# Optimization experiments

Hardware: AMD Instinct MI355X
Metric: run time of the kernel (lower is better)

Reference implementation:

```python
import jax, jax.numpy as jnp
import numpy as np
from jax import lax
from jax.scipy.special import ndtri
from jax.scipy.stats import norm

# Hyperparameters from __init__ defaults (num_inputs=8)
MU_A = 0.99          # sigmoid(logit_mu_a)
SIGMA_A = 0.1
A_MAX = 1.0          # truncation upper bound (module-level constant in repo)
SIGMASQ0 = 1.0       # initial-state variance (module-level constant in repo)
SIGMA_MU_X = 1.0
MU_W = 0.0
SIGMA_W = 1.0

S, T, D = 512, 8192, 8


def setup_inputs() -> dict:
    key = jax.random.key(0)
    ks = jax.random.split(key, 8)
    return dict(
        inputs=jax.random.normal(ks[0], (S, T, D), jnp.float32),
        eps_w=jax.random.normal(ks[1], (S, D), jnp.float32),
        u_a=jax.random.uniform(ks[2], (S,), jnp.float32, 1e-4, 1.0 - 1e-4),
        sigmasq=jax.random.uniform(ks[3], (S,), jnp.float32, 0.01, 0.3),
        eps_mu=jax.random.normal(ks[4], (S,), jnp.float32),
        eps_x0=jax.random.normal(ks[5], (S,), jnp.float32),
        eps_x=jax.random.normal(ks[6], (S, T), jnp.float32),
        u_bern=jax.random.uniform(ks[7], (S, T), jnp.float32),
    )


def reference(inputs, eps_w, u_a, sigmasq, eps_mu, eps_x0, eps_x, u_bern):
    # Per-subject parameter draws (reparameterized)
    w = MU_W + SIGMA_W * eps_w                              # [S, D]  Normal(mu_w, sigma_w)
    # TruncatedNormal(MU_A, SIGMA_A, 0, A_MAX) via inverse CDF
    alpha = (0.0 - MU_A) / SIGMA_A
    beta = (A_MAX - MU_A) / SIGMA_A
    Fa, Fb = norm.cdf(alpha), norm.cdf(beta)
    a = MU_A + SIGMA_A * ndtri(Fa + u_a * (Fb - Fa))        # [S]
    mu_x = SIGMA_MU_X * eps_mu                              # [S]  Normal(0, sigma_mu_x)
    b = mu_x * (1.0 - a)                                    # [S]
    x0 = mu_x + jnp.sqrt(SIGMASQ0) * eps_x0                 # [S]
    sd = jnp.sqrt(sigmasq)                                  # [S]

    # AR(1) latent scan over trials, vectorized over subjects.
    # Matches original: outputs collect x_t BEFORE the update, i.e. x_0..x_{T-1}.
    def step(x, eps_t):
        x_next = a * x + b + sd * eps_t
        return x_next, x

    _, xs = lax.scan(step, x0, eps_x.T)                     # xs: [T, S]
    x = xs.T                                                # [S, T]

    logits = x + jnp.einsum('std,sd->st', inputs, w)        # [S, T]
    y = (u_bern < jax.nn.sigmoid(logits)).astype(jnp.int32) # Bernoulli(logits) sample
    return x, y
```

## Files before the change

### kernel.cpp

```cpp
#include <hip/hip_runtime.h>
#include <cmath>

#define S_SUB 512
#define T_TR  8192
#define D_IN  8
#define NSEG  4
#define SEGT  (T_TR/NSEG)
#define BLK   256
#define CH    (SEGT/BLK)
#define NW    (BLK/64)

typedef float f4 __attribute__((ext_vector_type(4)));

__device__ __forceinline__ void param_chain(double Fa, double dF,
    float ua, float sq, float emu, float ex0,
    double& a, double& b, double& sd, double& x0)
{
    const double RS2 = 0.7071067811865476;
    const double S2  = 1.4142135623730951;
    const double ISQ = 0.3989422804014327;
    double p = fma((double)ua, dF, Fa);
    double z = -S2 * erfcinv(2.0 * p);
    #pragma unroll
    for (int it = 0; it < 2; ++it) {
        double F   = 0.5 * erfc(-z * RS2);
        double pdf = exp(-0.5 * z * z) * ISQ;
        z -= (F - p) / pdf;
    }
    a  = 0.99 + 0.1 * z;
    double mu = (double)emu;
    b  = mu * (1.0 - a);
    x0 = mu + (double)ex0;
    sd = sqrt((double)sq);
}

__global__ __launch_bounds__(BLK) void compose_kernel(
    const float* __restrict__ eps_x,
    const float* __restrict__ u_a,
    const float* __restrict__ sigmasq,
    const float* __restrict__ eps_mu,
    const float* __restrict__ eps_x0,
    double Fa, double dF,
    double2* __restrict__ comp,
    double* __restrict__ params)
{
    const int bid = blockIdx.x;
    const int s   = bid >> 2;
    const int seg = bid & 3;
    if (seg == NSEG - 1) return;
    const int tid  = threadIdx.x;
    const int lane = tid & 63;
    const int wid  = tid >> 6;

    __shared__ double  pl[3];
    __shared__ double2 wtot[NW];

    const size_t base = (size_t)s * T_TR + (size_t)seg * SEGT + (size_t)tid * CH;

    const f4* e4 = (const f4*)(eps_x + base);
    f4 v0 = e4[0];
    f4 v1 = e4[1];

    if (tid < 64) {
        double a, b, sd, x0;
        param_chain(Fa, dF, u_a[s], sigmasq[s], eps_mu[s], eps_x0[s], a, b, sd, x0);
        if (tid == 0) {
            pl[0] = a; pl[1] = b; pl[2] = sd;
            if (seg == 0) {
                params[4*s+0] = a;  params[4*s+1] = b;
                params[4*s+2] = sd; params[4*s+3] = x0;
            }
        }
    }
    __syncthreads();
    const double a = pl[0], b = pl[1], sd = pl[2];

    float ev[CH];
    ev[0]=v0.x; ev[1]=v0.y; ev[2]=v0.z; ev[3]=v0.w;
    ev[4]=v1.x; ev[5]=v1.y; ev[6]=v1.z; ev[7]=v1.w;

    double A = 1.0, Bv = 0.0;
    #pragma unroll
    for (int j = 0; j < CH; ++j) {
        double c = fma(sd, (double)ev[j], b);
        Bv = fma(a, Bv, c);
        A *= a;
    }

    #pragma unroll
    for (int off = 1; off < 64; off <<= 1) {
        double pA = __shfl_down(A, off);
        double pB = __shfl_down(Bv, off);
        Bv = fma(pA, Bv, pB);
        A  = pA * A;
    }
    if (lane == 0) wtot[wid] = make_double2(A, Bv);
    __syncthreads();
    if (tid == 0) {
        double CA = wtot[0].x, CB = wtot[0].y;
        #pragma unroll
        for (int w = 1; w < NW; ++w) {
            CB = fma(wtot[w].x, CB, wtot[w].y);
            CA = wtot[w].x * CA;
        }
        comp[seg * S_SUB + s] = make_double2(CA, CB);
    }
}

__global__ __launch_bounds__(BLK, 8) void fused_kernel(
    const float* __restrict__ inputs,
    const float* __restrict__ eps_w,
    const float* __restrict__ eps_x,
    const float* __restrict__ u_bern,
    const double* __restrict__ params,
    const double2* __restrict__ comp,
    float* __restrict__ out_x,
    float* __restrict__ out_y)
{
    const int bid  = blockIdx.x;
    const int s    = bid >> 2;
    const int seg  = bid & 3;
    const int tid  = threadIdx.x;
    const int lane = tid & 63;
    const int wid  = tid >> 6;

    __shared__ double2 wtot[NW];
    __shared__ double  xs[BLK * (CH + 1)];

    const size_t segbase = (size_t)s * T_TR + (size_t)seg * SEGT;
    const size_t base    = segbase + (size_t)tid * CH;

    const f4* e4 = (const f4*)(eps_x + base);
    f4 ev0 = e4[0];
    f4 ev1 = e4[1];

    const double a  = params[4*s+0];
    const double b  = params[4*s+1];
    const double sd = params[4*s+2];
    double xseed    = params[4*s+3];
    for (int i = 0; i < seg; ++i) {
        double2 c = comp[i * S_SUB + s];
        xseed = fma(c.x, xseed, c.y);
    }

    const float* wp = eps_w + s * D_IN;
    const double w0 = (double)wp[0], w1 = (double)wp[1];
    const double w2 = (double)wp[2], w3 = (double)wp[3];
    const double w4 = (double)wp[4], w5 = (double)wp[5];
    const double w6 = (double)wp[6], w7 = (double)wp[7];

    float ev[CH];
    ev[0]=ev0.x; ev[1]=ev0.y; ev[2]=ev0.z; ev[3]=ev0.w;
    ev[4]=ev1.x; ev[5]=ev1.y; ev[6]=ev1.z; ev[7]=ev1.w;

    double A = 1.0, Bv = 0.0;
    #pragma unroll
    for (int j = 0; j < CH; ++j) {
        double c = fma(sd, (double)ev[j], b);
        Bv = fma(a, Bv, c);
        A *= a;
    }

    #pragma unroll
    for (int off = 1; off < 64; off <<= 1) {
        double pA = __shfl_up(A, off);
        double pB = __shfl_up(Bv, off);
        if (lane >= off) {
            Bv = fma(A, pB, Bv);
            A  = A * pA;
        }
    }
    if (lane == 63) wtot[wid] = make_double2(A, Bv);
    __syncthreads();

    double PA = 1.0, PB = 0.0;
    for (int w = 0; w < wid; ++w) {
        double2 t = wtot[w];
        PB = fma(t.x, PB, t.y);
        PA = t.x * PA;
    }
    double eA = __shfl_up(A, 1);
    double eB = __shfl_up(Bv, 1);
    if (lane == 0) { eA = 1.0; eB = 0.0; }
    double EB = fma(eA, PB, eB);
    double EA = eA * PA;
    double x  = fma(EA, xseed, EB);

    #pragma unroll
    for (int j = 0; j < CH; ++j) {
        xs[tid * (CH + 1) + j] = x;
        double c = fma(sd, (double)ev[j], b);
        x = fma(a, x, c);
    }
    __syncthreads();

    float uv[CH];
    #pragma unroll
    for (int j = 0; j < CH; ++j)
        uv[j] = u_bern[segbase + j * BLK + tid];

    const f4* in4 = (const f4*)(inputs + segbase * D_IN);
    #pragma unroll
    for (int j = 0; j < CH; ++j) {
        const int t = j * BLK + tid;
        f4 i0 = in4[2*t];
        f4 i1 = in4[2*t + 1];
        double xv = xs[(t >> 3) * (CH + 1) + (t & 7)];
        double dot = fma((double)i0.x, w0,
                     fma((double)i0.y, w1,
                     fma((double)i0.z, w2,
                     fma((double)i0.w, w3,
                     fma((double)i1.x, w4,
                     fma((double)i1.y, w5,
                     fma((double)i1.z, w6, (double)i1.w * w7)))))));
        double L = xv + dot;
        double E = exp(-L);
        out_y[segbase + t] = ((double)uv[j] * (1.0 + E) < 1.0) ? 1.0f : 0.0f;
        out_x[segbase + t] = (float)xv;
    }
}

extern "C" void kernel_launch(void* const* d_in, const int* in_sizes, int n_in,
                              void* d_out, int out_size, void* d_ws, size_t ws_size,
                              hipStream_t stream) {
    const float* inputs  = (const float*)d_in[0];
    const float* eps_w   = (const float*)d_in[1];
    const float* u_a     = (const float*)d_in[2];
    const float* sigmasq = (const float*)d_in[3];
    const float* eps_mu  = (const float*)d_in[4];
    const float* eps_x0  = (const float*)d_in[5];
    const float* eps_x   = (const float*)d_in[6];
    const float* u_bern  = (const float*)d_in[7];

    float* out = (float*)d_out;

    double*  params = (double*)d_ws;
    double2* comp   = (double2*)((char*)d_ws + 16*1024);

    const double RS2 = 0.7071067811865476;
    const double Fa  = 0.5 * erfc(9.9 * RS2);
    const double Fb  = 0.5 * erfc(-0.1 * RS2);
    const double dF  = Fb - Fa;

    compose_kernel<<<S_SUB*NSEG, BLK, 0, stream>>>(eps_x, u_a, sigmasq, eps_mu,
                                                   eps_x0, Fa, dF, comp, params);
    fused_kernel<<<S_SUB*NSEG, BLK, 0, stream>>>(inputs, eps_w, eps_x, u_bern,
                                                 params, comp,
                                                 out, out + (size_t)S_SUB * T_TR);
}
```

Before: 41.12 us.

## Fold segment-carry composition into main kernel, move param setup to tiny kernel

Replaces the compose kernel, which launched 2048 blocks to reduce earlier segments, with a small setup kernel that only computes per-subject AR parameters. The main kernel now recomputes the composed affine transform of all preceding segments itself, by reading their eps_x slices and doing a block reduction. This removes a large kernel launch and the comp workspace round-trip. In exchange, later segments redo up to three segments' worth of reads and reductions, plus extra block barriers, so work is uneven across blocks.

```diff
diff --git a/kernel.cpp b/kernel.cpp
--- a/kernel.cpp
+++ b/kernel.cpp
@@ -12,14 +12,18 @@
 
 typedef float f4 __attribute__((ext_vector_type(4)));
 
-__device__ __forceinline__ void param_chain(double Fa, double dF,
-    float ua, float sq, float emu, float ex0,
-    double& a, double& b, double& sd, double& x0)
-{
+__global__ void setup_kernel(const float* __restrict__ u_a,
+                             const float* __restrict__ sigmasq,
+                             const float* __restrict__ eps_mu,
+                             const float* __restrict__ eps_x0,
+                             double Fa, double dF,
+                             double* __restrict__ params) {
+    int s = blockIdx.x * blockDim.x + threadIdx.x;
+    if (s >= S_SUB) return;
     const double RS2 = 0.7071067811865476;
     const double S2  = 1.4142135623730951;
     const double ISQ = 0.3989422804014327;
-    double p = fma((double)ua, dF, Fa);
+    double p = fma((double)u_a[s], dF, Fa);
     double z = -S2 * erfcinv(2.0 * p);
     #pragma unroll
     for (int it = 0; it < 2; ++it) {
@@ -27,93 +31,23 @@
         double pdf = exp(-0.5 * z * z) * ISQ;
         z -= (F - p) / pdf;
     }
-    a  = 0.99 + 0.1 * z;
-    double mu = (double)emu;
-    b  = mu * (1.0 - a);
-    x0 = mu + (double)ex0;
-    sd = sqrt((double)sq);
+    double a  = 0.99 + 0.1 * z;
+    double mu = (double)eps_mu[s];
+    double b  = mu * (1.0 - a);
+    double x0 = mu + (double)eps_x0[s];
+    double sd = sqrt((double)sigmasq[s]);
+    params[4*s+0] = a;
+    params[4*s+1] = b;
+    params[4*s+2] = sd;
+    params[4*s+3] = x0;
 }
 
-__global__ __launch_bounds__(BLK) void compose_kernel(
-    const float* __restrict__ eps_x,
-    const float* __restrict__ u_a,
-    const float* __restrict__ sigmasq,
-    const float* __restrict__ eps_mu,
-    const float* __restrict__ eps_x0,
-    double Fa, double dF,
-    double2* __restrict__ comp,
-    double* __restrict__ params)
-{
-    const int bid = blockIdx.x;
-    const int s   = bid >> 2;
-    const int seg = bid & 3;
-    if (seg == NSEG - 1) return;
-    const int tid  = threadIdx.x;
-    const int lane = tid & 63;
-    const int wid  = tid >> 6;
-
-    __shared__ double  pl[3];
-    __shared__ double2 wtot[NW];
-
-    const size_t base = (size_t)s * T_TR + (size_t)seg * SEGT + (size_t)tid * CH;
-
-    const f4* e4 = (const f4*)(eps_x + base);
-    f4 v0 = e4[0];
-    f4 v1 = e4[1];
-
-    if (tid < 64) {
-        double a, b, sd, x0;
-        param_chain(Fa, dF, u_a[s], sigmasq[s], eps_mu[s], eps_x0[s], a, b, sd, x0);
-        if (tid == 0) {
-            pl[0] = a; pl[1] = b; pl[2] = sd;
-            if (seg == 0) {
-                params[4*s+0] = a;  params[4*s+1] = b;
-                params[4*s+2] = sd; params[4*s+3] = x0;
-            }
-        }
-    }
-    __syncthreads();
-    const double a = pl[0], b = pl[1], sd = pl[2];
-
-    float ev[CH];
-    ev[0]=v0.x; ev[1]=v0.y; ev[2]=v0.z; ev[3]=v0.w;
-    ev[4]=v1.x; ev[5]=v1.y; ev[6]=v1.z; ev[7]=v1.w;
-
-    double A = 1.0, Bv = 0.0;
-    #pragma unroll
-    for (int j = 0; j < CH; ++j) {
-        double c = fma(sd, (double)ev[j], b);
-        Bv = fma(a, Bv, c);
-        A *= a;
-    }
-
-    #pragma unroll
-    for (int off = 1; off < 64; off <<= 1) {
-        double pA = __shfl_down(A, off);
-        double pB = __shfl_down(Bv, off);
-        Bv = fma(pA, Bv, pB);
-        A  = pA * A;
-    }
-    if (lane == 0) wtot[wid] = make_double2(A, Bv);
-    __syncthreads();
-    if (tid == 0) {
-        double CA = wtot[0].x, CB = wtot[0].y;
-        #pragma unroll
-        for (int w = 1; w < NW; ++w) {
-            CB = fma(wtot[w].x, CB, wtot[w].y);
-            CA = wtot[w].x * CA;
-        }
-        comp[seg * S_SUB + s] = make_double2(CA, CB);
-    }
-}
-
-__global__ __launch_bounds__(BLK, 8) void fused_kernel(
+__global__ __launch_bounds__(BLK, 8) void mono_kernel(
     const float* __restrict__ inputs,
     const float* __restrict__ eps_w,
     const float* __restrict__ eps_x,
     const float* __restrict__ u_bern,
     const double* __restrict__ params,
-    const double2* __restrict__ comp,
     float* __restrict__ out_x,
     float* __restrict__ out_y)
 {
@@ -127,31 +61,65 @@
     __shared__ double2 wtot[NW];
     __shared__ double  xs[BLK * (CH + 1)];
 
-    const size_t segbase = (size_t)s * T_TR + (size_t)seg * SEGT;
-    const size_t base    = segbase + (size_t)tid * CH;
+    const size_t subjbase = (size_t)s * T_TR;
+    const size_t segbase  = subjbase + (size_t)seg * SEGT;
+    const size_t base     = segbase + (size_t)tid * CH;
 
     const f4* e4 = (const f4*)(eps_x + base);
-    f4 ev0 = e4[0];
-    f4 ev1 = e4[1];
+    f4 o0 = e4[0];
+    f4 o1 = e4[1];
+    f4 q0[3], q1[3];
+    #pragma unroll
+    for (int p = 0; p < NSEG - 1; ++p) {
+        if (p < seg) {
+            const f4* ep = (const f4*)(eps_x + subjbase + (size_t)p * SEGT
+                                       + (size_t)tid * CH);
+            q0[p] = ep[0];
+            q1[p] = ep[1];
+        }
+    }
 
     const double a  = params[4*s+0];
     const double b  = params[4*s+1];
     const double sd = params[4*s+2];
     double xseed    = params[4*s+3];
-    for (int i = 0; i < seg; ++i) {
-        double2 c = comp[i * S_SUB + s];
-        xseed = fma(c.x, xseed, c.y);
-    }
-
-    const float* wp = eps_w + s * D_IN;
-    const double w0 = (double)wp[0], w1 = (double)wp[1];
-    const double w2 = (double)wp[2], w3 = (double)wp[3];
-    const double w4 = (double)wp[4], w5 = (double)wp[5];
-    const double w6 = (double)wp[6], w7 = (double)wp[7];
+
+    #pragma unroll
+    for (int p = 0; p < NSEG - 1; ++p) {
+        if (p < seg) {
+            float evp[CH];
+            evp[0]=q0[p].x; evp[1]=q0[p].y; evp[2]=q0[p].z; evp[3]=q0[p].w;
+            evp[4]=q1[p].x; evp[5]=q1[p].y; evp[6]=q1[p].z; evp[7]=q1[p].w;
+            double A = 1.0, Bv = 0.0;
+            #pragma unroll
+            for (int j = 0; j < CH; ++j) {
+                double c = fma(sd, (double)evp[j], b);
+                Bv = fma(a, Bv, c);
+                A *= a;
+            }
+            #pragma unroll
+            for (int off = 1; off < 64; off <<= 1) {
+                double pA = __shfl_down(A, off);
+                double pB = __shfl_down(Bv, off);
+                Bv = fma(pA, Bv, pB);
+                A  = pA * A;
+            }
+            if (lane == 0) wtot[wid] = make_double2(A, Bv);
+            __syncthreads();
+            double CA = wtot[0].x, CB = wtot[0].y;
+            #pragma unroll
+            for (int w = 1; w < NW; ++w) {
+                CB = fma(wtot[w].x, CB, wtot[w].y);
+                CA = wtot[w].x * CA;
+            }
+            xseed = fma(CA, xseed, CB);
+            __syncthreads();
+        }
+    }
 
     float ev[CH];
-    ev[0]=ev0.x; ev[1]=ev0.y; ev[2]=ev0.z; ev[3]=ev0.w;
-    ev[4]=ev1.x; ev[5]=ev1.y; ev[6]=ev1.z; ev[7]=ev1.w;
+    ev[0]=o0.x; ev[1]=o0.y; ev[2]=o0.z; ev[3]=o0.w;
+    ev[4]=o1.x; ev[5]=o1.y; ev[6]=o1.z; ev[7]=o1.w;
 
     double A = 1.0, Bv = 0.0;
     #pragma unroll
@@ -160,7 +128,6 @@
         Bv = fma(a, Bv, c);
         A *= a;
     }
-
     #pragma unroll
     for (int off = 1; off < 64; off <<= 1) {
         double pA = __shfl_up(A, off);
@@ -193,6 +160,12 @@
         x = fma(a, x, c);
     }
     __syncthreads();
+
+    const float* wp = eps_w + s * D_IN;
+    const double w0 = (double)wp[0], w1 = (double)wp[1];
+    const double w2 = (double)wp[2], w3 = (double)wp[3];
+    const double w4 = (double)wp[4], w5 = (double)wp[5];
+    const double w6 = (double)wp[6], w7 = (double)wp[7];
 
     float uv[CH];
     #pragma unroll
@@ -232,19 +205,16 @@
     const float* eps_x   = (const float*)d_in[6];
     const float* u_bern  = (const float*)d_in[7];
 
-    float* out = (float*)d_out;
-
-    double*  params = (double*)d_ws;
-    double2* comp   = (double2*)((char*)d_ws + 16*1024);
+    float*  out    = (float*)d_out;
+    double* params = (double*)d_ws;
 
     const double RS2 = 0.7071067811865476;
     const double Fa  = 0.5 * erfc(9.9 * RS2);
     const double Fb  = 0.5 * erfc(-0.1 * RS2);
     const double dF  = Fb - Fa;
 
-    compose_kernel<<<S_SUB*NSEG, BLK, 0, stream>>>(eps_x, u_a, sigmasq, eps_mu,
-                                                   eps_x0, Fa, dF, comp, params);
-    fused_kernel<<<S_SUB*NSEG, BLK, 0, stream>>>(inputs, eps_w, eps_x, u_bern,
-                                                 params, comp,
-                                                 out, out + (size_t)S_SUB * T_TR);
+    setup_kernel<<<2, 256, 0, stream>>>(u_a, sigmasq, eps_mu, eps_x0, Fa, dF, params);
+    mono_kernel<<<S_SUB*NSEG, BLK, 0, stream>>>(inputs, eps_w, eps_x, u_bern,
+                                                params,
+                                                out, out + (size_t)S_SUB * T_TR);
 }
```

Result: slower. 43.93 us (+6.9%).
